# Kernel optimization log

Measured on AMD Instinct MI355X. Metric: run time of the kernel, lower is better.

Reference implementation:

```python
import jax, jax.numpy as jnp
import numpy as np

N, K_, D_ = 16384, 32, 128

def setup_inputs() -> dict:
    key = jax.random.key(0)
    k1, k2, k3 = jax.random.split(key, 3)
    x = jax.random.normal(k1, (1, N, D_), dtype=jnp.float32)
    codes = jax.random.normal(k2, (K_, D_), dtype=jnp.float32)
    scale = jax.random.uniform(k3, (K_,), dtype=jnp.float32)
    return {"x": x, "codes": codes, "scale": scale}

def reference(x, codes, scale):
    # x: (1, N, D) -> residuals R: (N, K, D)
    R = x[0][:, None, :] - codes[None, :, :]
    # scaled L2 norm (NOT squared) over D, scaled per-codeword by `scale`
    l2 = jnp.linalg.norm(R, axis=-1)            # (N, K)
    W = jax.nn.softmax(l2 * scale, axis=-1)     # softmax over K
    # aggregated encoding: (K, D)
    E = jnp.einsum('nk,nkd->kd', W, R)
    return E
```

## Files before the change

kernel.cpp:

```cpp
#include <hip/hip_runtime.h>

constexpr int N    = 16384;
constexpr int K    = 32;
constexpr int D    = 128;
constexpr int SPAD = K + 2;

template <int CTRL>
__device__ __forceinline__ float dpp_add(float v) {
    int j = __builtin_amdgcn_update_dpp(0, __float_as_int(v), CTRL, 0xF, 0xF, false);
    return v + __int_as_float(j);
}
__device__ __forceinline__ float sum16(float v) {
    v = dpp_add<0xB1>(v);
    v = dpp_add<0x4E>(v);
    v = dpp_add<0x141>(v);
    v = dpp_add<0x140>(v);
    return v;
}

constexpr int ROWS1 = 8;
constexpr int GRID1 = N / ROWS1;

__global__ __launch_bounds__(256) void enc_partial(
    const float* __restrict__ x,
    const float* __restrict__ codes,
    const float* __restrict__ scale,
    float* __restrict__ ws)
{
    __shared__ float sc_lds[ROWS1][SPAD];
    __shared__ float w_lds[ROWS1][SPAD];

    const int tid = threadIdx.x;
    const int kg  = tid >> 4;
    const int dg  = tid & 15;
    const int d4  = dg << 2;
    const int k0  = kg << 1;

    const float* xb = x + (long)blockIdx.x * ROWS1 * D;
    float4 xr[ROWS1][2];
    #pragma unroll
    for (int n = 0; n < ROWS1; ++n) {
        xr[n][0] = *reinterpret_cast<const float4*>(xb + n * D + d4);
        xr[n][1] = *reinterpret_cast<const float4*>(xb + n * D + 64 + d4);
    }

    const float4 cA0 = *reinterpret_cast<const float4*>(&codes[k0 * D + d4]);
    const float4 cA1 = *reinterpret_cast<const float4*>(&codes[k0 * D + 64 + d4]);
    const float4 cB0 = *reinterpret_cast<const float4*>(&codes[(k0 + 1) * D + d4]);
    const float4 cB1 = *reinterpret_cast<const float4*>(&codes[(k0 + 1) * D + 64 + d4]);
    const float sA = scale[k0];
    const float sB = scale[k0 + 1];

    #pragma unroll
    for (int n = 0; n < ROWS1; ++n) {
        const float4 xa = xr[n][0];
        const float4 xb4 = xr[n][1];
        float r;
        float pA0 = 0.f, pA1 = 0.f, pB0 = 0.f, pB1 = 0.f;
        r = xa.x - cA0.x;  pA0 = fmaf(r, r, pA0);
        r = xa.y - cA0.y;  pA1 = fmaf(r, r, pA1);
        r = xa.z - cA0.z;  pA0 = fmaf(r, r, pA0);
        r = xa.w - cA0.w;  pA1 = fmaf(r, r, pA1);
        r = xb4.x - cA1.x; pA0 = fmaf(r, r, pA0);
        r = xb4.y - cA1.y; pA1 = fmaf(r, r, pA1);
        r = xb4.z - cA1.z; pA0 = fmaf(r, r, pA0);
        r = xb4.w - cA1.w; pA1 = fmaf(r, r, pA1);
        r = xa.x - cB0.x;  pB0 = fmaf(r, r, pB0);
        r = xa.y - cB0.y;  pB1 = fmaf(r, r, pB1);
        r = xa.z - cB0.z;  pB0 = fmaf(r, r, pB0);
        r = xa.w - cB0.w;  pB1 = fmaf(r, r, pB1);
        r = xb4.x - cB1.x; pB0 = fmaf(r, r, pB0);
        r = xb4.y - cB1.y; pB1 = fmaf(r, r, pB1);
        r = xb4.z - cB1.z; pB0 = fmaf(r, r, pB0);
        r = xb4.w - cB1.w; pB1 = fmaf(r, r, pB1);
        float pA = sum16(pA0 + pA1);
        float pB = sum16(pB0 + pB1);
        if (dg == 0) {
            sc_lds[n][k0]     = sqrtf(pA) * sA;
            sc_lds[n][k0 + 1] = sqrtf(pB) * sB;
        }
    }
    __syncthreads();

    {
        const int row = tid >> 5;
        const int q   = tid & 31;
        float s = sc_lds[row][q];
        float m = s;
        m = fmaxf(m, __shfl_xor(m, 1));
        m = fmaxf(m, __shfl_xor(m, 2));
        m = fmaxf(m, __shfl_xor(m, 4));
        m = fmaxf(m, __shfl_xor(m, 8));
        m = fmaxf(m, __shfl_xor(m, 16));
        const float LOG2E = 1.44269504088896f;
        float e = exp2f((s - m) * LOG2E);
        float sum = e;
        sum += __shfl_xor(sum, 1);
        sum += __shfl_xor(sum, 2);
        sum += __shfl_xor(sum, 4);
        sum += __shfl_xor(sum, 8);
        sum += __shfl_xor(sum, 16);
        w_lds[row][q] = e * (1.0f / sum);
    }
    __syncthreads();

    float4 tA0 = make_float4(0.f, 0.f, 0.f, 0.f);
    float4 tA1 = tA0, tB0 = tA0, tB1 = tA0;
    float swA = 0.f, swB = 0.f;
    #pragma unroll
    for (int n = 0; n < ROWS1; ++n) {
        const float2 w = *reinterpret_cast<const float2*>(&w_lds[n][k0]);
        const float4 xa = xr[n][0];
        const float4 xb4 = xr[n][1];
        tA0.x = fmaf(w.x, xa.x, tA0.x);
        tA0.y = fmaf(w.x, xa.y, tA0.y);
        tA0.z = fmaf(w.x, xa.z, tA0.z);
        tA0.w = fmaf(w.x, xa.w, tA0.w);
        tA1.x = fmaf(w.x, xb4.x, tA1.x);
        tA1.y = fmaf(w.x, xb4.y, tA1.y);
        tA1.z = fmaf(w.x, xb4.z, tA1.z);
        tA1.w = fmaf(w.x, xb4.w, tA1.w);
        tB0.x = fmaf(w.y, xa.x, tB0.x);
        tB0.y = fmaf(w.y, xa.y, tB0.y);
        tB0.z = fmaf(w.y, xa.z, tB0.z);
        tB0.w = fmaf(w.y, xa.w, tB0.w);
        tB1.x = fmaf(w.y, xb4.x, tB1.x);
        tB1.y = fmaf(w.y, xb4.y, tB1.y);
        tB1.z = fmaf(w.y, xb4.z, tB1.z);
        tB1.w = fmaf(w.y, xb4.w, tB1.w);
        swA += w.x;
        swB += w.y;
    }

    float* o = ws + (long)blockIdx.x * (K * D) + k0 * D + d4;
    *reinterpret_cast<float4*>(o)       = make_float4(tA0.x - swA * cA0.x, tA0.y - swA * cA0.y,
                                                      tA0.z - swA * cA0.z, tA0.w - swA * cA0.w);
    *reinterpret_cast<float4*>(o + 64)  = make_float4(tA1.x - swA * cA1.x, tA1.y - swA * cA1.y,
                                                      tA1.z - swA * cA1.z, tA1.w - swA * cA1.w);
    *reinterpret_cast<float4*>(o + 128) = make_float4(tB0.x - swB * cB0.x, tB0.y - swB * cB0.y,
                                                      tB0.z - swB * cB0.z, tB0.w - swB * cB0.w);
    *reinterpret_cast<float4*>(o + 192) = make_float4(tB1.x - swB * cB1.x, tB1.y - swB * cB1.y,
                                                      tB1.z - swB * cB1.z, tB1.w - swB * cB1.w);
}

__global__ __launch_bounds__(256) void reduce2(
    const float* __restrict__ ws, float* __restrict__ out)
{
    __shared__ float4 part[32][8];

    const int tid   = threadIdx.x;
    const int col   = tid & 7;
    const int slice = tid >> 3;
    const int gcol  = blockIdx.x * 8 + col;

    const float4* P = reinterpret_cast<const float4*>(ws);
    float4 acc = make_float4(0.f, 0.f, 0.f, 0.f);
    #pragma unroll 8
    for (int r = 0; r < 64; ++r) {
        float4 v = P[(long)(slice * 64 + r) * 1024 + gcol];
        acc.x += v.x; acc.y += v.y; acc.z += v.z; acc.w += v.w;
    }
    part[slice][col] = acc;
    __syncthreads();

    #pragma unroll
    for (int stride = 16; stride >= 1; stride >>= 1) {
        if (tid < stride * 8) {
            float4 a = part[slice][col];
            float4 b = part[slice + stride][col];
            a.x += b.x; a.y += b.y; a.z += b.z; a.w += b.w;
            part[slice][col] = a;
        }
        __syncthreads();
    }
    if (tid < 8) {
        reinterpret_cast<float4*>(out)[blockIdx.x * 8 + tid] = part[0][tid];
    }
}

constexpr int ROWSF = 64;
constexpr int FPAD  = K + 4;

__global__ __launch_bounds__(256) void enc_atomic(
    const float* __restrict__ x,
    const float* __restrict__ codes,
    const float* __restrict__ scale,
    float* __restrict__ out)
{
    __shared__ float sc_lds[ROWSF][FPAD];
    __shared__ float w_lds[ROWSF][FPAD];

    const int tid = threadIdx.x;
    const int k   = tid >> 3;
    const int dc  = tid & 7;
    const int d0  = dc << 4;

    const float4 ck0 = *reinterpret_cast<const float4*>(&codes[k * D + d0 + 0]);
    const float4 ck1 = *reinterpret_cast<const float4*>(&codes[k * D + d0 + 4]);
    const float4 ck2 = *reinterpret_cast<const float4*>(&codes[k * D + d0 + 8]);
    const float4 ck3 = *reinterpret_cast<const float4*>(&codes[k * D + d0 + 12]);
    const float scl = scale[k];

    const float* xb = x + (long)blockIdx.x * ROWSF * D + d0;

    #pragma unroll 4
    for (int n = 0; n < ROWSF; ++n) {
        const float4* xr = reinterpret_cast<const float4*>(xb + (long)n * D);
        float4 x0 = xr[0], x1 = xr[1], x2 = xr[2], x3 = xr[3];
        float p = 0.f, r;
        r = x0.x - ck0.x; p = fmaf(r, r, p);
        r = x0.y - ck0.y; p = fmaf(r, r, p);
        r = x0.z - ck0.z; p = fmaf(r, r, p);
        r = x0.w - ck0.w; p = fmaf(r, r, p);
        r = x1.x - ck1.x; p = fmaf(r, r, p);
        r = x1.y - ck1.y; p = fmaf(r, r, p);
        r = x1.z - ck1.z; p = fmaf(r, r, p);
        r = x1.w - ck1.w; p = fmaf(r, r, p);
        r = x2.x - ck2.x; p = fmaf(r, r, p);
        r = x2.y - ck2.y; p = fmaf(r, r, p);
        r = x2.z - ck2.z; p = fmaf(r, r, p);
        r = x2.w - ck2.w; p = fmaf(r, r, p);
        r = x3.x - ck3.x; p = fmaf(r, r, p);
        r = x3.y - ck3.y; p = fmaf(r, r, p);
        r = x3.z - ck3.z; p = fmaf(r, r, p);
        r = x3.w - ck3.w; p = fmaf(r, r, p);
        p += __shfl_xor(p, 1);
        p += __shfl_xor(p, 2);
        p += __shfl_xor(p, 4);
        if (dc == 0) sc_lds[n][k] = sqrtf(p) * scl;
    }
    __syncthreads();

    {
        const int row = tid >> 2;
        const int q   = tid & 3;
        float4 s0 = *reinterpret_cast<const float4*>(&sc_lds[row][q * 8 + 0]);
        float4 s1 = *reinterpret_cast<const float4*>(&sc_lds[row][q * 8 + 4]);
        float m = fmaxf(fmaxf(fmaxf(s0.x, s0.y), fmaxf(s0.z, s0.w)),
                        fmaxf(fmaxf(s1.x, s1.y), fmaxf(s1.z, s1.w)));
        m = fmaxf(m, __shfl_xor(m, 1));
        m = fmaxf(m, __shfl_xor(m, 2));
        const float LOG2E = 1.44269504088896f;
        float e0 = exp2f((s0.x - m) * LOG2E);
        float e1 = exp2f((s0.y - m) * LOG2E);
        float e2 = exp2f((s0.z - m) * LOG2E);
        float e3 = exp2f((s0.w - m) * LOG2E);
        float e4 = exp2f((s1.x - m) * LOG2E);
        float e5 = exp2f((s1.y - m) * LOG2E);
        float e6 = exp2f((s1.z - m) * LOG2E);
        float e7 = exp2f((s1.w - m) * LOG2E);
        float sum = ((e0 + e1) + (e2 + e3)) + ((e4 + e5) + (e6 + e7));
        sum += __shfl_xor(sum, 1);
        sum += __shfl_xor(sum, 2);
        float inv = 1.0f / sum;
        *reinterpret_cast<float4*>(&w_lds[row][q * 8 + 0]) =
            make_float4(e0 * inv, e1 * inv, e2 * inv, e3 * inv);
        *reinterpret_cast<float4*>(&w_lds[row][q * 8 + 4]) =
            make_float4(e4 * inv, e5 * inv, e6 * inv, e7 * inv);
    }
    __syncthreads();

    float4 t0 = make_float4(0.f, 0.f, 0.f, 0.f);
    float4 t1 = t0, t2 = t0, t3 = t0;
    float sw = 0.f;
    #pragma unroll 4
    for (int n = 0; n < ROWSF; ++n) {
        float w = w_lds[n][k];
        const float4* xr = reinterpret_cast<const float4*>(xb + (long)n * D);
        float4 x0 = xr[0], x1 = xr[1], x2 = xr[2], x3 = xr[3];
        t0.x = fmaf(w, x0.x, t0.x);
        t0.y = fmaf(w, x0.y, t0.y);
        t0.z = fmaf(w, x0.z, t0.z);
        t0.w = fmaf(w, x0.w, t0.w);
        t1.x = fmaf(w, x1.x, t1.x);
        t1.y = fmaf(w, x1.y, t1.y);
        t1.z = fmaf(w, x1.z, t1.z);
        t1.w = fmaf(w, x1.w, t1.w);
        t2.x = fmaf(w, x2.x, t2.x);
        t2.y = fmaf(w, x2.y, t2.y);
        t2.z = fmaf(w, x2.z, t2.z);
        t2.w = fmaf(w, x2.w, t2.w);
        t3.x = fmaf(w, x3.x, t3.x);
        t3.y = fmaf(w, x3.y, t3.y);
        t3.z = fmaf(w, x3.z, t3.z);
        t3.w = fmaf(w, x3.w, t3.w);
        sw += w;
    }

    float* o = out + k * D + d0;
    atomicAdd(&o[0],  t0.x - sw * ck0.x);
    atomicAdd(&o[1],  t0.y - sw * ck0.y);
    atomicAdd(&o[2],  t0.z - sw * ck0.z);
    atomicAdd(&o[3],  t0.w - sw * ck0.w);
    atomicAdd(&o[4],  t1.x - sw * ck1.x);
    atomicAdd(&o[5],  t1.y - sw * ck1.y);
    atomicAdd(&o[6],  t1.z - sw * ck1.z);
    atomicAdd(&o[7],  t1.w - sw * ck1.w);
    atomicAdd(&o[8],  t2.x - sw * ck2.x);
    atomicAdd(&o[9],  t2.y - sw * ck2.y);
    atomicAdd(&o[10], t2.z - sw * ck2.z);
    atomicAdd(&o[11], t2.w - sw * ck2.w);
    atomicAdd(&o[12], t3.x - sw * ck3.x);
    atomicAdd(&o[13], t3.y - sw * ck3.y);
    atomicAdd(&o[14], t3.z - sw * ck3.z);
    atomicAdd(&o[15], t3.w - sw * ck3.w);
}

extern "C" void kernel_launch(void* const* d_in, const int* in_sizes, int n_in,
                              void* d_out, int out_size, void* d_ws, size_t ws_size,
                              hipStream_t stream) {
    const float* x     = (const float*)d_in[0];
    const float* codes = (const float*)d_in[1];
    const float* scale = (const float*)d_in[2];
    float* out = (float*)d_out;

    const size_t ws_needed = (size_t)GRID1 * K * D * sizeof(float);
    if (ws_size >= ws_needed) {
        float* ws = (float*)d_ws;
        enc_partial<<<GRID1, 256, 0, stream>>>(x, codes, scale, ws);
        reduce2<<<128, 256, 0, stream>>>(ws, out);
    } else {
        hipMemsetAsync(out, 0, K * D * sizeof(float), stream);
        enc_atomic<<<N / ROWSF, 256, 0, stream>>>(x, codes, scale, out);
    }
}
```

Before: 29.73 us.

## Fuse partial encoding and reduction into one cooperative kernel with grid sync

Adds a cooperative kernel that has 512 blocks each process 32 rows in chunks of 8, write per-block partials to the workspace, then perform a grid-wide sync and reduce the partials within the same kernel. This replaces the two-launch partial/reduce path, shrinking the workspace traffic from 2048 partial slabs to 512 and removing the second launch. It costs a grid barrier and relies on cooperative launch succeeding, falling back to the old path otherwise. The atomic fallback kernel is removed, so when the workspace is too small no output is produced.

Result: slower. 91.05 us (+206.2%).

```diff
diff --git a/kernel.cpp b/kernel.cpp
--- a/kernel.cpp
+++ b/kernel.cpp
@@ -1,4 +1,7 @@
 #include <hip/hip_runtime.h>
+#include <hip/hip_cooperative_groups.h>
+
+namespace cg = cooperative_groups;
 
 constexpr int N    = 16384;
 constexpr int K    = 32;
@@ -16,6 +19,173 @@
     v = dpp_add<0x141>(v);
     v = dpp_add<0x140>(v);
     return v;
+}
+
+constexpr int CGRID  = 512;
+constexpr int CROWS  = N / CGRID;
+constexpr int CHUNK  = 8;
+constexpr int NCHUNK = CROWS / CHUNK;
+
+__global__ __launch_bounds__(256, 2) void enc_coop(
+    const float* __restrict__ x,
+    const float* __restrict__ codes,
+    const float* __restrict__ scale,
+    float* __restrict__ ws,
+    float* __restrict__ out)
+{
+    __shared__ float sc_lds[CHUNK][SPAD];
+    __shared__ float w_lds[CHUNK][SPAD];
+    __shared__ float4 part[128][2];
+
+    const int tid = threadIdx.x;
+    const int kg  = tid >> 4;
+    const int dg  = tid & 15;
+    const int d4  = dg << 2;
+    const int k0  = kg << 1;
+
+    const float4 cA0 = *reinterpret_cast<const float4*>(&codes[k0 * D + d4]);
+    const float4 cA1 = *reinterpret_cast<const float4*>(&codes[k0 * D + 64 + d4]);
+    const float4 cB0 = *reinterpret_cast<const float4*>(&codes[(k0 + 1) * D + d4]);
+    const float4 cB1 = *reinterpret_cast<const float4*>(&codes[(k0 + 1) * D + 64 + d4]);
+    const float sA = scale[k0];
+    const float sB = scale[k0 + 1];
+
+    float4 tA0 = make_float4(0.f, 0.f, 0.f, 0.f);
+    float4 tA1 = tA0, tB0 = tA0, tB1 = tA0;
+    float swA = 0.f, swB = 0.f;
+
+    const float* xb = x + (long)blockIdx.x * CROWS * D;
+
+    for (int c = 0; c < NCHUNK; ++c) {
+        float4 xr[CHUNK][2];
+        const float* xc = xb + c * CHUNK * D;
+        #pragma unroll
+        for (int n = 0; n < CHUNK; ++n) {
+            xr[n][0] = *reinterpret_cast<const float4*>(xc + n * D + d4);
+            xr[n][1] = *reinterpret_cast<const float4*>(xc + n * D + 64 + d4);
+        }
+
+        #pragma unroll
+        for (int n = 0; n < CHUNK; ++n) {
+            const float4 xa = xr[n][0];
+            const float4 xb4 = xr[n][1];
+            float r;
+            float pA0 = 0.f, pA1 = 0.f, pB0 = 0.f, pB1 = 0.f;
+            r = xa.x - cA0.x;  pA0 = fmaf(r, r, pA0);
+            r = xa.y - cA0.y;  pA1 = fmaf(r, r, pA1);
+            r = xa.z - cA0.z;  pA0 = fmaf(r, r, pA0);
+            r = xa.w - cA0.w;  pA1 = fmaf(r, r, pA1);
+            r = xb4.x - cA1.x; pA0 = fmaf(r, r, pA0);
+            r = xb4.y - cA1.y; pA1 = fmaf(r, r, pA1);
+            r = xb4.z - cA1.z; pA0 = fmaf(r, r, pA0);
+            r = xb4.w - cA1.w; pA1 = fmaf(r, r, pA1);
+            r = xa.x - cB0.x;  pB0 = fmaf(r, r, pB0);
+            r = xa.y - cB0.y;  pB1 = fmaf(r, r, pB1);
+            r = xa.z - cB0.z;  pB0 = fmaf(r, r, pB0);
+            r = xa.w - cB0.w;  pB1 = fmaf(r, r, pB1);
+            r = xb4.x - cB1.x; pB0 = fmaf(r, r, pB0);
+            r = xb4.y - cB1.y; pB1 = fmaf(r, r, pB1);
+            r = xb4.z - cB1.z; pB0 = fmaf(r, r, pB0);
+            r = xb4.w - cB1.w; pB1 = fmaf(r, r, pB1);
+            float pA = sum16(pA0 + pA1);
+            float pB = sum16(pB0 + pB1);
+            if (dg == 0) {
+                sc_lds[n][k0]     = sqrtf(pA) * sA;
+                sc_lds[n][k0 + 1] = sqrtf(pB) * sB;
+            }
+        }
+        __syncthreads();
+
+        {
+            const int row = tid >> 5;
+            const int q   = tid & 31;
+            float s = sc_lds[row][q];
+            float m = s;
+            m = fmaxf(m, __shfl_xor(m, 1));
+            m = fmaxf(m, __shfl_xor(m, 2));
+            m = fmaxf(m, __shfl_xor(m, 4));
+            m = fmaxf(m, __shfl_xor(m, 8));
+            m = fmaxf(m, __shfl_xor(m, 16));
+            const float LOG2E = 1.44269504088896f;
+            float e = exp2f((s - m) * LOG2E);
+            float sum = e;
+            sum += __shfl_xor(sum, 1);
+            sum += __shfl_xor(sum, 2);
+            sum += __shfl_xor(sum, 4);
+            sum += __shfl_xor(sum, 8);
+            sum += __shfl_xor(sum, 16);
+            w_lds[row][q] = e * (1.0f / sum);
+        }
+        __syncthreads();
+
+        #pragma unroll
+        for (int n = 0; n < CHUNK; ++n) {
+            const float2 w = *reinterpret_cast<const float2*>(&w_lds[n][k0]);
+            const float4 xa = xr[n][0];
+            const float4 xb4 = xr[n][1];
+            tA0.x = fmaf(w.x, xa.x, tA0.x);
+            tA0.y = fmaf(w.x, xa.y, tA0.y);
+            tA0.z = fmaf(w.x, xa.z, tA0.z);
+            tA0.w = fmaf(w.x, xa.w, tA0.w);
+            tA1.x = fmaf(w.x, xb4.x, tA1.x);
+            tA1.y = fmaf(w.x, xb4.y, tA1.y);
+            tA1.z = fmaf(w.x, xb4.z, tA1.z);
+            tA1.w = fmaf(w.x, xb4.w, tA1.w);
+            tB0.x = fmaf(w.y, xa.x, tB0.x);
+            tB0.y = fmaf(w.y, xa.y, tB0.y);
+            tB0.z = fmaf(w.y, xa.z, tB0.z);
+            tB0.w = fmaf(w.y, xa.w, tB0.w);
+            tB1.x = fmaf(w.y, xb4.x, tB1.x);
+            tB1.y = fmaf(w.y, xb4.y, tB1.y);
+            tB1.z = fmaf(w.y, xb4.z, tB1.z);
+            tB1.w = fmaf(w.y, xb4.w, tB1.w);
+            swA += w.x;
+            swB += w.y;
+        }
+        __syncthreads();
+    }
+
+    {
+        float* o = ws + (long)blockIdx.x * (K * D) + k0 * D + d4;
+        *reinterpret_cast<float4*>(o)       = make_float4(tA0.x - swA * cA0.x, tA0.y - swA * cA0.y,
+                                                          tA0.z - swA * cA0.z, tA0.w - swA * cA0.w);
+        *reinterpret_cast<float4*>(o + 64)  = make_float4(tA1.x - swA * cA1.x, tA1.y - swA * cA1.y,
+                                                          tA1.z - swA * cA1.z, tA1.w - swA * cA1.w);
+        *reinterpret_cast<float4*>(o + 128) = make_float4(tB0.x - swB * cB0.x, tB0.y - swB * cB0.y,
+                                                          tB0.z - swB * cB0.z, tB0.w - swB * cB0.w);
+        *reinterpret_cast<float4*>(o + 192) = make_float4(tB1.x - swB * cB1.x, tB1.y - swB * cB1.y,
+                                                          tB1.z - swB * cB1.z, tB1.w - swB * cB1.w);
+    }
+
+    cg::this_grid().sync();
+
+    {
+        const int col   = tid & 1;
+        const int slice = tid >> 1;
+        const int gcol  = blockIdx.x * 2 + col;
+        const float4* P = reinterpret_cast<const float4*>(ws);
+        float4 acc = make_float4(0.f, 0.f, 0.f, 0.f);
+        #pragma unroll
+        for (int r = 0; r < 4; ++r) {
+            float4 v = P[(long)(slice * 4 + r) * 1024 + gcol];
+            acc.x += v.x; acc.y += v.y; acc.z += v.z; acc.w += v.w;
+        }
+        part[slice][col] = acc;
+        __syncthreads();
+        #pragma unroll
+        for (int stride = 64; stride >= 1; stride >>= 1) {
+            if (tid < stride * 2) {
+                float4 a = part[slice][col];
+                float4 b = part[slice + stride][col];
+                a.x += b.x; a.y += b.y; a.z += b.z; a.w += b.w;
+                part[slice][col] = a;
+            }
+            __syncthreads();
+        }
+        if (tid < 2) {
+            reinterpret_cast<float4*>(out)[blockIdx.x * 2 + tid] = part[0][tid];
+        }
+    }
 }
 
 constexpr int ROWS1 = 8;
@@ -178,134 +348,6 @@
     }
 }
 
-constexpr int ROWSF = 64;
-constexpr int FPAD  = K + 4;
-
-__global__ __launch_bounds__(256) void enc_atomic(
-    const float* __restrict__ x,
-    const float* __restrict__ codes,
-    const float* __restrict__ scale,
-    float* __restrict__ out)
-{
-    __shared__ float sc_lds[ROWSF][FPAD];
-    __shared__ float w_lds[ROWSF][FPAD];
-
-    const int tid = threadIdx.x;
-    const int k   = tid >> 3;
-    const int dc  = tid & 7;
-    const int d0  = dc << 4;
-
-    const float4 ck0 = *reinterpret_cast<const float4*>(&codes[k * D + d0 + 0]);
-    const float4 ck1 = *reinterpret_cast<const float4*>(&codes[k * D + d0 + 4]);
-    const float4 ck2 = *reinterpret_cast<const float4*>(&codes[k * D + d0 + 8]);
-    const float4 ck3 = *reinterpret_cast<const float4*>(&codes[k * D + d0 + 12]);
-    const float scl = scale[k];
-
-    const float* xb = x + (long)blockIdx.x * ROWSF * D + d0;
-
-    #pragma unroll 4
-    for (int n = 0; n < ROWSF; ++n) {
-        const float4* xr = reinterpret_cast<const float4*>(xb + (long)n * D);
-        float4 x0 = xr[0], x1 = xr[1], x2 = xr[2], x3 = xr[3];
-        float p = 0.f, r;
-        r = x0.x - ck0.x; p = fmaf(r, r, p);
-        r = x0.y - ck0.y; p = fmaf(r, r, p);
-        r = x0.z - ck0.z; p = fmaf(r, r, p);
-        r = x0.w - ck0.w; p = fmaf(r, r, p);
-        r = x1.x - ck1.x; p = fmaf(r, r, p);
-        r = x1.y - ck1.y; p = fmaf(r, r, p);
-        r = x1.z - ck1.z; p = fmaf(r, r, p);
-        r = x1.w - ck1.w; p = fmaf(r, r, p);
-        r = x2.x - ck2.x; p = fmaf(r, r, p);
-        r = x2.y - ck2.y; p = fmaf(r, r, p);
-        r = x2.z - ck2.z; p = fmaf(r, r, p);
-        r = x2.w - ck2.w; p = fmaf(r, r, p);
-        r = x3.x - ck3.x; p = fmaf(r, r, p);
-        r = x3.y - ck3.y; p = fmaf(r, r, p);
-        r = x3.z - ck3.z; p = fmaf(r, r, p);
-        r = x3.w - ck3.w; p = fmaf(r, r, p);
-        p += __shfl_xor(p, 1);
-        p += __shfl_xor(p, 2);
-        p += __shfl_xor(p, 4);
-        if (dc == 0) sc_lds[n][k] = sqrtf(p) * scl;
-    }
-    __syncthreads();
-
-    {
-        const int row = tid >> 2;
-        const int q   = tid & 3;
-        float4 s0 = *reinterpret_cast<const float4*>(&sc_lds[row][q * 8 + 0]);
-        float4 s1 = *reinterpret_cast<const float4*>(&sc_lds[row][q * 8 + 4]);
-        float m = fmaxf(fmaxf(fmaxf(s0.x, s0.y), fmaxf(s0.z, s0.w)),
-                        fmaxf(fmaxf(s1.x, s1.y), fmaxf(s1.z, s1.w)));
-        m = fmaxf(m, __shfl_xor(m, 1));
-        m = fmaxf(m, __shfl_xor(m, 2));
-        const float LOG2E = 1.44269504088896f;
-        float e0 = exp2f((s0.x - m) * LOG2E);
-        float e1 = exp2f((s0.y - m) * LOG2E);
-        float e2 = exp2f((s0.z - m) * LOG2E);
-        float e3 = exp2f((s0.w - m) * LOG2E);
-        float e4 = exp2f((s1.x - m) * LOG2E);
-        float e5 = exp2f((s1.y - m) * LOG2E);
-        float e6 = exp2f((s1.z - m) * LOG2E);
-        float e7 = exp2f((s1.w - m) * LOG2E);
-        float sum = ((e0 + e1) + (e2 + e3)) + ((e4 + e5) + (e6 + e7));
-        sum += __shfl_xor(sum, 1);
-        sum += __shfl_xor(sum, 2);
-        float inv = 1.0f / sum;
-        *reinterpret_cast<float4*>(&w_lds[row][q * 8 + 0]) =
-            make_float4(e0 * inv, e1 * inv, e2 * inv, e3 * inv);
-        *reinterpret_cast<float4*>(&w_lds[row][q * 8 + 4]) =
-            make_float4(e4 * inv, e5 * inv, e6 * inv, e7 * inv);
-    }
-    __syncthreads();
-
-    float4 t0 = make_float4(0.f, 0.f, 0.f, 0.f);
-    float4 t1 = t0, t2 = t0, t3 = t0;
-    float sw = 0.f;
-    #pragma unroll 4
-    for (int n = 0; n < ROWSF; ++n) {
-        float w = w_lds[n][k];
-        const float4* xr = reinterpret_cast<const float4*>(xb + (long)n * D);
-        float4 x0 = xr[0], x1 = xr[1], x2 = xr[2], x3 = xr[3];
-        t0.x = fmaf(w, x0.x, t0.x);
-        t0.y = fmaf(w, x0.y, t0.y);
-        t0.z = fmaf(w, x0.z, t0.z);
-        t0.w = fmaf(w, x0.w, t0.w);
-        t1.x = fmaf(w, x1.x, t1.x);
-        t1.y = fmaf(w, x1.y, t1.y);
-        t1.z = fmaf(w, x1.z, t1.z);
-        t1.w = fmaf(w, x1.w, t1.w);
-        t2.x = fmaf(w, x2.x, t2.x);
-        t2.y = fmaf(w, x2.y, t2.y);
-        t2.z = fmaf(w, x2.z, t2.z);
-        t2.w = fmaf(w, x2.w, t2.w);
-        t3.x = fmaf(w, x3.x, t3.x);
-        t3.y = fmaf(w, x3.y, t3.y);
-        t3.z = fmaf(w, x3.z, t3.z);
-        t3.w = fmaf(w, x3.w, t3.w);
-        sw += w;
-    }
-
-    float* o = out + k * D + d0;
-    atomicAdd(&o[0],  t0.x - sw * ck0.x);
-    atomicAdd(&o[1],  t0.y - sw * ck0.y);
-    atomicAdd(&o[2],  t0.z - sw * ck0.z);
-    atomicAdd(&o[3],  t0.w - sw * ck0.w);
-    atomicAdd(&o[4],  t1.x - sw * ck1.x);
-    atomicAdd(&o[5],  t1.y - sw * ck1.y);
-    atomicAdd(&o[6],  t1.z - sw * ck1.z);
-    atomicAdd(&o[7],  t1.w - sw * ck1.w);
-    atomicAdd(&o[8],  t2.x - sw * ck2.x);
-    atomicAdd(&o[9],  t2.y - sw * ck2.y);
-    atomicAdd(&o[10], t2.z - sw * ck2.z);
-    atomicAdd(&o[11], t2.w - sw * ck2.w);
-    atomicAdd(&o[12], t3.x - sw * ck3.x);
-    atomicAdd(&o[13], t3.y - sw * ck3.y);
-    atomicAdd(&o[14], t3.z - sw * ck3.z);
-    atomicAdd(&o[15], t3.w - sw * ck3.w);
-}
-
 extern "C" void kernel_launch(void* const* d_in, const int* in_sizes, int n_in,
                               void* d_out, int out_size, void* d_ws, size_t ws_size,
                               hipStream_t stream) {
@@ -313,14 +355,19 @@
     const float* codes = (const float*)d_in[1];
     const float* scale = (const float*)d_in[2];
     float* out = (float*)d_out;
+    float* ws  = (float*)d_ws;
+
+    const size_t ws_coop = (size_t)CGRID * K * D * sizeof(float);
+    if (ws_size >= ws_coop) {
+        void* args[] = { (void*)&x, (void*)&codes, (void*)&scale, (void*)&ws, (void*)&out };
+        hipError_t err = hipLaunchCooperativeKernel(
+            reinterpret_cast<void*>(enc_coop), dim3(CGRID), dim3(256), args, 0, stream);
+        if (err == hipSuccess) return;
+    }
 
     const size_t ws_needed = (size_t)GRID1 * K * D * sizeof(float);
     if (ws_size >= ws_needed) {
-        float* ws = (float*)d_ws;
         enc_partial<<<GRID1, 256, 0, stream>>>(x, codes, scale, ws);
         reduce2<<<128, 256, 0, stream>>>(ws, out);
-    } else {
-        hipMemsetAsync(out, 0, K * D * sizeof(float), stream);
-        enc_atomic<<<N / ROWSF, 256, 0, stream>>>(x, codes, scale, out);
-    }
-}
+    }
+}
```

## Loop row chunks per block to shrink partial workspace and reduction traffic

Applied to the files above, without the earlier changes.

The partial-encoding kernel now walks several 8-row chunks per block and keeps accumulators in registers, so the grid drops from 2048 to 512 blocks. That cuts the workspace written and re-read by the reduction kernel by four times. The reduction is widened to 256 blocks with 64 slices, and both kernels use nontemporal stores and loads for the workspace. The atomic fallback kernel is removed. In exchange each block runs serial chunks with three barriers per chunk, and the first kernel has fewer blocks to hide latency.

Result: no change. 29.26 us (-1.6%).

```diff
diff --git a/kernel.cpp b/kernel.cpp
--- a/kernel.cpp
+++ b/kernel.cpp
@@ -4,6 +4,8 @@
 constexpr int K    = 32;
 constexpr int D    = 128;
 constexpr int SPAD = K + 2;
+
+typedef float f4 __attribute__((ext_vector_type(4)));
 
 template <int CTRL>
 __device__ __forceinline__ float dpp_add(float v) {
@@ -18,31 +20,21 @@
     return v;
 }
 
-constexpr int ROWS1 = 8;
-constexpr int GRID1 = N / ROWS1;
-
 __global__ __launch_bounds__(256) void enc_partial(
     const float* __restrict__ x,
     const float* __restrict__ codes,
     const float* __restrict__ scale,
-    float* __restrict__ ws)
+    float* __restrict__ ws,
+    int nchunk)
 {
-    __shared__ float sc_lds[ROWS1][SPAD];
-    __shared__ float w_lds[ROWS1][SPAD];
+    __shared__ float sc_lds[8][SPAD];
+    __shared__ float w_lds[8][SPAD];
 
     const int tid = threadIdx.x;
     const int kg  = tid >> 4;
     const int dg  = tid & 15;
     const int d4  = dg << 2;
     const int k0  = kg << 1;
-
-    const float* xb = x + (long)blockIdx.x * ROWS1 * D;
-    float4 xr[ROWS1][2];
-    #pragma unroll
-    for (int n = 0; n < ROWS1; ++n) {
-        xr[n][0] = *reinterpret_cast<const float4*>(xb + n * D + d4);
-        xr[n][1] = *reinterpret_cast<const float4*>(xb + n * D + 64 + d4);
-    }
 
     const float4 cA0 = *reinterpret_cast<const float4*>(&codes[k0 * D + d4]);
     const float4 cA1 = *reinterpret_cast<const float4*>(&codes[k0 * D + 64 + d4]);
@@ -51,259 +43,147 @@
     const float sA = scale[k0];
     const float sB = scale[k0 + 1];
 
-    #pragma unroll
-    for (int n = 0; n < ROWS1; ++n) {
-        const float4 xa = xr[n][0];
-        const float4 xb4 = xr[n][1];
-        float r;
-        float pA0 = 0.f, pA1 = 0.f, pB0 = 0.f, pB1 = 0.f;
-        r = xa.x - cA0.x;  pA0 = fmaf(r, r, pA0);
-        r = xa.y - cA0.y;  pA1 = fmaf(r, r, pA1);
-        r = xa.z - cA0.z;  pA0 = fmaf(r, r, pA0);
-        r = xa.w - cA0.w;  pA1 = fmaf(r, r, pA1);
-        r = xb4.x - cA1.x; pA0 = fmaf(r, r, pA0);
-        r = xb4.y - cA1.y; pA1 = fmaf(r, r, pA1);
-        r = xb4.z - cA1.z; pA0 = fmaf(r, r, pA0);
-        r = xb4.w - cA1.w; pA1 = fmaf(r, r, pA1);
-        r = xa.x - cB0.x;  pB0 = fmaf(r, r, pB0);
-        r = xa.y - cB0.y;  pB1 = fmaf(r, r, pB1);
-        r = xa.z - cB0.z;  pB0 = fmaf(r, r, pB0);
-        r = xa.w - cB0.w;  pB1 = fmaf(r, r, pB1);
-        r = xb4.x - cB1.x; pB0 = fmaf(r, r, pB0);
-        r = xb4.y - cB1.y; pB1 = fmaf(r, r, pB1);
-        r = xb4.z - cB1.z; pB0 = fmaf(r, r, pB0);
-        r = xb4.w - cB1.w; pB1 = fmaf(r, r, pB1);
-        float pA = sum16(pA0 + pA1);
-        float pB = sum16(pB0 + pB1);
-        if (dg == 0) {
-            sc_lds[n][k0]     = sqrtf(pA) * sA;
-            sc_lds[n][k0 + 1] = sqrtf(pB) * sB;
-        }
-    }
-    __syncthreads();
-
-    {
-        const int row = tid >> 5;
-        const int q   = tid & 31;
-        float s = sc_lds[row][q];
-        float m = s;
-        m = fmaxf(m, __shfl_xor(m, 1));
-        m = fmaxf(m, __shfl_xor(m, 2));
-        m = fmaxf(m, __shfl_xor(m, 4));
-        m = fmaxf(m, __shfl_xor(m, 8));
-        m = fmaxf(m, __shfl_xor(m, 16));
-        const float LOG2E = 1.44269504088896f;
-        float e = exp2f((s - m) * LOG2E);
-        float sum = e;
-        sum += __shfl_xor(sum, 1);
-        sum += __shfl_xor(sum, 2);
-        sum += __shfl_xor(sum, 4);
-        sum += __shfl_xor(sum, 8);
-        sum += __shfl_xor(sum, 16);
-        w_lds[row][q] = e * (1.0f / sum);
-    }
-    __syncthreads();
-
     float4 tA0 = make_float4(0.f, 0.f, 0.f, 0.f);
     float4 tA1 = tA0, tB0 = tA0, tB1 = tA0;
     float swA = 0.f, swB = 0.f;
-    #pragma unroll
-    for (int n = 0; n < ROWS1; ++n) {
-        const float2 w = *reinterpret_cast<const float2*>(&w_lds[n][k0]);
-        const float4 xa = xr[n][0];
-        const float4 xb4 = xr[n][1];
-        tA0.x = fmaf(w.x, xa.x, tA0.x);
-        tA0.y = fmaf(w.x, xa.y, tA0.y);
-        tA0.z = fmaf(w.x, xa.z, tA0.z);
-        tA0.w = fmaf(w.x, xa.w, tA0.w);
-        tA1.x = fmaf(w.x, xb4.x, tA1.x);
-        tA1.y = fmaf(w.x, xb4.y, tA1.y);
-        tA1.z = fmaf(w.x, xb4.z, tA1.z);
-        tA1.w = fmaf(w.x, xb4.w, tA1.w);
-        tB0.x = fmaf(w.y, xa.x, tB0.x);
-        tB0.y = fmaf(w.y, xa.y, tB0.y);
-        tB0.z = fmaf(w.y, xa.z, tB0.z);
-        tB0.w = fmaf(w.y, xa.w, tB0.w);
-        tB1.x = fmaf(w.y, xb4.x, tB1.x);
-        tB1.y = fmaf(w.y, xb4.y, tB1.y);
-        tB1.z = fmaf(w.y, xb4.z, tB1.z);
-        tB1.w = fmaf(w.y, xb4.w, tB1.w);
-        swA += w.x;
-        swB += w.y;
-    }
-
-    float* o = ws + (long)blockIdx.x * (K * D) + k0 * D + d4;
-    *reinterpret_cast<float4*>(o)       = make_float4(tA0.x - swA * cA0.x, tA0.y - swA * cA0.y,
-                                                      tA0.z - swA * cA0.z, tA0.w - swA * cA0.w);
-    *reinterpret_cast<float4*>(o + 64)  = make_float4(tA1.x - swA * cA1.x, tA1.y - swA * cA1.y,
-                                                      tA1.z - swA * cA1.z, tA1.w - swA * cA1.w);
-    *reinterpret_cast<float4*>(o + 128) = make_float4(tB0.x - swB * cB0.x, tB0.y - swB * cB0.y,
-                                                      tB0.z - swB * cB0.z, tB0.w - swB * cB0.w);
-    *reinterpret_cast<float4*>(o + 192) = make_float4(tB1.x - swB * cB1.x, tB1.y - swB * cB1.y,
-                                                      tB1.z - swB * cB1.z, tB1.w - swB * cB1.w);
+
+    const float* xb = x + (long)blockIdx.x * nchunk * 8 * D;
+
+    for (int c = 0; c < nchunk; ++c) {
+        float4 xr[8][2];
+        const float* xc = xb + c * 8 * D;
+        #pragma unroll
+        for (int n = 0; n < 8; ++n) {
+            xr[n][0] = *reinterpret_cast<const float4*>(xc + n * D + d4);
+            xr[n][1] = *reinterpret_cast<const float4*>(xc + n * D + 64 + d4);
+        }
+
+        #pragma unroll
+        for (int n = 0; n < 8; ++n) {
+            const float4 xa = xr[n][0];
+            const float4 xb4 = xr[n][1];
+            float r;
+            float pA0 = 0.f, pA1 = 0.f, pB0 = 0.f, pB1 = 0.f;
+            r = xa.x - cA0.x;  pA0 = fmaf(r, r, pA0);
+            r = xa.y - cA0.y;  pA1 = fmaf(r, r, pA1);
+            r = xa.z - cA0.z;  pA0 = fmaf(r, r, pA0);
+            r = xa.w - cA0.w;  pA1 = fmaf(r, r, pA1);
+            r = xb4.x - cA1.x; pA0 = fmaf(r, r, pA0);
+            r = xb4.y - cA1.y; pA1 = fmaf(r, r, pA1);
+            r = xb4.z - cA1.z; pA0 = fmaf(r, r, pA0);
+            r = xb4.w - cA1.w; pA1 = fmaf(r, r, pA1);
+            r = xa.x - cB0.x;  pB0 = fmaf(r, r, pB0);
+            r = xa.y - cB0.y;  pB1 = fmaf(r, r, pB1);
+            r = xa.z - cB0.z;  pB0 = fmaf(r, r, pB0);
+            r = xa.w - cB0.w;  pB1 = fmaf(r, r, pB1);
+            r = xb4.x - cB1.x; pB0 = fmaf(r, r, pB0);
+            r = xb4.y - cB1.y; pB1 = fmaf(r, r, pB1);
+            r = xb4.z - cB1.z; pB0 = fmaf(r, r, pB0);
+            r = xb4.w - cB1.w; pB1 = fmaf(r, r, pB1);
+            float pA = sum16(pA0 + pA1);
+            float pB = sum16(pB0 + pB1);
+            if (dg == 0) {
+                sc_lds[n][k0]     = sqrtf(pA) * sA;
+                sc_lds[n][k0 + 1] = sqrtf(pB) * sB;
+            }
+        }
+        __syncthreads();
+
+        {
+            const int row = tid >> 5;
+            const int q   = tid & 31;
+            float s = sc_lds[row][q];
+            float m = s;
+            m = fmaxf(m, __shfl_xor(m, 1));
+            m = fmaxf(m, __shfl_xor(m, 2));
+            m = fmaxf(m, __shfl_xor(m, 4));
+            m = fmaxf(m, __shfl_xor(m, 8));
+            m = fmaxf(m, __shfl_xor(m, 16));
+            const float LOG2E = 1.44269504088896f;
+            float e = exp2f((s - m) * LOG2E);
+            float sum = e;
+            sum += __shfl_xor(sum, 1);
+            sum += __shfl_xor(sum, 2);
+            sum += __shfl_xor(sum, 4);
+            sum += __shfl_xor(sum, 8);
+            sum += __shfl_xor(sum, 16);
+            w_lds[row][q] = e * (1.0f / sum);
+        }
+        __syncthreads();
+
+        #pragma unroll
+        for (int n = 0; n < 8; ++n) {
+            const float2 w = *reinterpret_cast<const float2*>(&w_lds[n][k0]);
+            const float4 xa = xr[n][0];
+            const float4 xb4 = xr[n][1];
+            tA0.x = fmaf(w.x, xa.x, tA0.x);
+            tA0.y = fmaf(w.x, xa.y, tA0.y);
+            tA0.z = fmaf(w.x, xa.z, tA0.z);
+            tA0.w = fmaf(w.x, xa.w, tA0.w);
+            tA1.x = fmaf(w.x, xb4.x, tA1.x);
+            tA1.y = fmaf(w.x, xb4.y, tA1.y);
+            tA1.z = fmaf(w.x, xb4.z, tA1.z);
+            tA1.w = fmaf(w.x, xb4.w, tA1.w);
+            tB0.x = fmaf(w.y, xa.x, tB0.x);
+            tB0.y = fmaf(w.y, xa.y, tB0.y);
+            tB0.z = fmaf(w.y, xa.z, tB0.z);
+            tB0.w = fmaf(w.y, xa.w, tB0.w);
+            tB1.x = fmaf(w.y, xb4.x, tB1.x);
+            tB1.y = fmaf(w.y, xb4.y, tB1.y);
+            tB1.z = fmaf(w.y, xb4.z, tB1.z);
+            tB1.w = fmaf(w.y, xb4.w, tB1.w);
+            swA += w.x;
+            swB += w.y;
+        }
+        __syncthreads();
+    }
+
+    f4* o = reinterpret_cast<f4*>(ws + (long)blockIdx.x * (K * D) + k0 * D + d4);
+    f4 e0 = { tA0.x - swA * cA0.x, tA0.y - swA * cA0.y,
+              tA0.z - swA * cA0.z, tA0.w - swA * cA0.w };
+    f4 e1 = { tA1.x - swA * cA1.x, tA1.y - swA * cA1.y,
+              tA1.z - swA * cA1.z, tA1.w - swA * cA1.w };
+    f4 e2 = { tB0.x - swB * cB0.x, tB0.y - swB * cB0.y,
+              tB0.z - swB * cB0.z, tB0.w - swB * cB0.w };
+    f4 e3 = { tB1.x - swB * cB1.x, tB1.y - swB * cB1.y,
+              tB1.z - swB * cB1.z, tB1.w - swB * cB1.w };
+    __builtin_nontemporal_store(e0, o);
+    __builtin_nontemporal_store(e1, o + 16);
+    __builtin_nontemporal_store(e2, o + 32);
+    __builtin_nontemporal_store(e3, o + 48);
 }
 
 __global__ __launch_bounds__(256) void reduce2(
-    const float* __restrict__ ws, float* __restrict__ out)
+    const float* __restrict__ ws, float* __restrict__ out, int nrows)
 {
-    __shared__ float4 part[32][8];
+    __shared__ f4 part[64][4];
 
     const int tid   = threadIdx.x;
-    const int col   = tid & 7;
-    const int slice = tid >> 3;
-    const int gcol  = blockIdx.x * 8 + col;
-
-    const float4* P = reinterpret_cast<const float4*>(ws);
-    float4 acc = make_float4(0.f, 0.f, 0.f, 0.f);
-    #pragma unroll 8
-    for (int r = 0; r < 64; ++r) {
-        float4 v = P[(long)(slice * 64 + r) * 1024 + gcol];
-        acc.x += v.x; acc.y += v.y; acc.z += v.z; acc.w += v.w;
+    const int col   = tid & 3;
+    const int slice = tid >> 2;
+    const int gcol  = blockIdx.x * 4 + col;
+    const int rpt   = nrows >> 6;
+
+    const f4* P = reinterpret_cast<const f4*>(ws);
+    f4 acc = { 0.f, 0.f, 0.f, 0.f };
+    long base = (long)slice * rpt * 1024 + gcol;
+    for (int r = 0; r < rpt; ++r) {
+        f4 v = __builtin_nontemporal_load(P + base + (long)r * 1024);
+        acc += v;
     }
     part[slice][col] = acc;
     __syncthreads();
 
     #pragma unroll
-    for (int stride = 16; stride >= 1; stride >>= 1) {
-        if (tid < stride * 8) {
-            float4 a = part[slice][col];
-            float4 b = part[slice + stride][col];
-            a.x += b.x; a.y += b.y; a.z += b.z; a.w += b.w;
-            part[slice][col] = a;
-        }
-        __syncthreads();
-    }
-    if (tid < 8) {
-        reinterpret_cast<float4*>(out)[blockIdx.x * 8 + tid] = part[0][tid];
-    }
-}
-
-constexpr int ROWSF = 64;
-constexpr int FPAD  = K + 4;
-
-__global__ __launch_bounds__(256) void enc_atomic(
-    const float* __restrict__ x,
-    const float* __restrict__ codes,
-    const float* __restrict__ scale,
-    float* __restrict__ out)
-{
-    __shared__ float sc_lds[ROWSF][FPAD];
-    __shared__ float w_lds[ROWSF][FPAD];
-
-    const int tid = threadIdx.x;
-    const int k   = tid >> 3;
-    const int dc  = tid & 7;
-    const int d0  = dc << 4;
-
-    const float4 ck0 = *reinterpret_cast<const float4*>(&codes[k * D + d0 + 0]);
-    const float4 ck1 = *reinterpret_cast<const float4*>(&codes[k * D + d0 + 4]);
-    const float4 ck2 = *reinterpret_cast<const float4*>(&codes[k * D + d0 + 8]);
-    const float4 ck3 = *reinterpret_cast<const float4*>(&codes[k * D + d0 + 12]);
-    const float scl = scale[k];
-
-    const float* xb = x + (long)blockIdx.x * ROWSF * D + d0;
-
-    #pragma unroll 4
-    for (int n = 0; n < ROWSF; ++n) {
-        const float4* xr = reinterpret_cast<const float4*>(xb + (long)n * D);
-        float4 x0 = xr[0], x1 = xr[1], x2 = xr[2], x3 = xr[3];
-        float p = 0.f, r;
-        r = x0.x - ck0.x; p = fmaf(r, r, p);
-        r = x0.y - ck0.y; p = fmaf(r, r, p);
-        r = x0.z - ck0.z; p = fmaf(r, r, p);
-        r = x0.w - ck0.w; p = fmaf(r, r, p);
-        r = x1.x - ck1.x; p = fmaf(r, r, p);
-        r = x1.y - ck1.y; p = fmaf(r, r, p);
-        r = x1.z - ck1.z; p = fmaf(r, r, p);
-        r = x1.w - ck1.w; p = fmaf(r, r, p);
-        r = x2.x - ck2.x; p = fmaf(r, r, p);
-        r = x2.y - ck2.y; p = fmaf(r, r, p);
-        r = x2.z - ck2.z; p = fmaf(r, r, p);
-        r = x2.w - ck2.w; p = fmaf(r, r, p);
-        r = x3.x - ck3.x; p = fmaf(r, r, p);
-        r = x3.y - ck3.y; p = fmaf(r, r, p);
-        r = x3.z - ck3.z; p = fmaf(r, r, p);
-        r = x3.w - ck3.w; p = fmaf(r, r, p);
-        p += __shfl_xor(p, 1);
-        p += __shfl_xor(p, 2);
-        p += __shfl_xor(p, 4);
-        if (dc == 0) sc_lds[n][k] = sqrtf(p) * scl;
-    }
-    __syncthreads();
-
-    {
-        const int row = tid >> 2;
-        const int q   = tid & 3;
-        float4 s0 = *reinterpret_cast<const float4*>(&sc_lds[row][q * 8 + 0]);
-        float4 s1 = *reinterpret_cast<const float4*>(&sc_lds[row][q * 8 + 4]);
-        float m = fmaxf(fmaxf(fmaxf(s0.x, s0.y), fmaxf(s0.z, s0.w)),
-                        fmaxf(fmaxf(s1.x, s1.y), fmaxf(s1.z, s1.w)));
-        m = fmaxf(m, __shfl_xor(m, 1));
-        m = fmaxf(m, __shfl_xor(m, 2));
-        const float LOG2E = 1.44269504088896f;
-        float e0 = exp2f((s0.x - m) * LOG2E);
-        float e1 = exp2f((s0.y - m) * LOG2E);
-        float e2 = exp2f((s0.z - m) * LOG2E);
-        float e3 = exp2f((s0.w - m) * LOG2E);
-        float e4 = exp2f((s1.x - m) * LOG2E);
-        float e5 = exp2f((s1.y - m) * LOG2E);
-        float e6 = exp2f((s1.z - m) * LOG2E);
-        float e7 = exp2f((s1.w - m) * LOG2E);
-        float sum = ((e0 + e1) + (e2 + e3)) + ((e4 + e5) + (e6 + e7));
-        sum += __shfl_xor(sum, 1);
-        sum += __shfl_xor(sum, 2);
-        float inv = 1.0f / sum;
-        *reinterpret_cast<float4*>(&w_lds[row][q * 8 + 0]) =
-            make_float4(e0 * inv, e1 * inv, e2 * inv, e3 * inv);
-        *reinterpret_cast<float4*>(&w_lds[row][q * 8 + 4]) =
-            make_float4(e4 * inv, e5 * inv, e6 * inv, e7 * inv);
-    }
-    __syncthreads();
-
-    float4 t0 = make_float4(0.f, 0.f, 0.f, 0.f);
-    float4 t1 = t0, t2 = t0, t3 = t0;
-    float sw = 0.f;
-    #pragma unroll 4
-    for (int n = 0; n < ROWSF; ++n) {
-        float w = w_lds[n][k];
-        const float4* xr = reinterpret_cast<const float4*>(xb + (long)n * D);
-        float4 x0 = xr[0], x1 = xr[1], x2 = xr[2], x3 = xr[3];
-        t0.x = fmaf(w, x0.x, t0.x);
-        t0.y = fmaf(w, x0.y, t0.y);
-        t0.z = fmaf(w, x0.z, t0.z);
-        t0.w = fmaf(w, x0.w, t0.w);
-        t1.x = fmaf(w, x1.x, t1.x);
-        t1.y = fmaf(w, x1.y, t1.y);
-        t1.z = fmaf(w, x1.z, t1.z);
-        t1.w = fmaf(w, x1.w, t1.w);
-        t2.x = fmaf(w, x2.x, t2.x);
-        t2.y = fmaf(w, x2.y, t2.y);
-        t2.z = fmaf(w, x2.z, t2.z);
-        t2.w = fmaf(w, x2.w, t2.w);
-        t3.x = fmaf(w, x3.x, t3.x);
-        t3.y = fmaf(w, x3.y, t3.y);
-        t3.z = fmaf(w, x3.z, t3.z);
-        t3.w = fmaf(w, x3.w, t3.w);
-        sw += w;
-    }
-
-    float* o = out + k * D + d0;
-    atomicAdd(&o[0],  t0.x - sw * ck0.x);
-    atomicAdd(&o[1],  t0.y - sw * ck0.y);
-    atomicAdd(&o[2],  t0.z - sw * ck0.z);
-    atomicAdd(&o[3],  t0.w - sw * ck0.w);
-    atomicAdd(&o[4],  t1.x - sw * ck1.x);
-    atomicAdd(&o[5],  t1.y - sw * ck1.y);
-    atomicAdd(&o[6],  t1.z - sw * ck1.z);
-    atomicAdd(&o[7],  t1.w - sw * ck1.w);
-    atomicAdd(&o[8],  t2.x - sw * ck2.x);
-    atomicAdd(&o[9],  t2.y - sw * ck2.y);
-    atomicAdd(&o[10], t2.z - sw * ck2.z);
-    atomicAdd(&o[11], t2.w - sw * ck2.w);
-    atomicAdd(&o[12], t3.x - sw * ck3.x);
-    atomicAdd(&o[13], t3.y - sw * ck3.y);
-    atomicAdd(&o[14], t3.z - sw * ck3.z);
-    atomicAdd(&o[15], t3.w - sw * ck3.w);
+    for (int stride = 32; stride >= 1; stride >>= 1) {
+        if (tid < stride * 4) {
+            part[slice][col] += part[slice + stride][col];
+        }
+        __syncthreads();
+    }
+    if (tid < 4) {
+        reinterpret_cast<f4*>(out)[blockIdx.x * 4 + tid] = part[0][tid];
+    }
 }
 
 extern "C" void kernel_launch(void* const* d_in, const int* in_sizes, int n_in,
@@ -313,14 +193,12 @@
     const float* codes = (const float*)d_in[1];
     const float* scale = (const float*)d_in[2];
     float* out = (float*)d_out;
-
-    const size_t ws_needed = (size_t)GRID1 * K * D * sizeof(float);
-    if (ws_size >= ws_needed) {
-        float* ws = (float*)d_ws;
-        enc_partial<<<GRID1, 256, 0, stream>>>(x, codes, scale, ws);
-        reduce2<<<128, 256, 0, stream>>>(ws, out);
-    } else {
-        hipMemsetAsync(out, 0, K * D * sizeof(float), stream);
-        enc_atomic<<<N / ROWSF, 256, 0, stream>>>(x, codes, scale, out);
-    }
-}
+    float* ws  = (float*)d_ws;
+
+    int grid1 = 512;
+    if (ws_size < (size_t)grid1 * K * D * sizeof(float)) grid1 = 128;
+    const int nchunk = N / (grid1 * 8);
+
+    enc_partial<<<grid1, 256, 0, stream>>>(x, codes, scale, ws, nchunk);
+    reduce2<<<256, 256, 0, stream>>>(ws, out, grid1);
+}
```
